# Performance work log

Hardware: AMD Instinct MI355X
Metric: run time of the kernel (lower is better)

## Reference

```python
import jax, jax.numpy as jnp
import numpy as np

INPUT_DIM = 1024
HIDDEN_DIM = 1024
FORGET_BIAS = 0.0


def setup_inputs() -> dict:
    key = jax.random.key(0)
    ks = jax.random.split(key, 8)
    x = jax.random.normal(ks[0], (1024, 32, INPUT_DIM), dtype=jnp.float32)
    state = jnp.zeros((1, 32, HIDDEN_DIM), dtype=jnp.float32)
    std = 0.1
    wm_z = std * jax.random.normal(ks[1], (HIDDEN_DIM, INPUT_DIM), dtype=jnp.float32)
    wm_f = std * jax.random.normal(ks[2], (HIDDEN_DIM, INPUT_DIM), dtype=jnp.float32)
    wv_z = std * jax.random.normal(ks[3], (1, HIDDEN_DIM), dtype=jnp.float32)
    wv_f = std * jax.random.normal(ks[4], (1, HIDDEN_DIM), dtype=jnp.float32)
    bias_z = std * jax.random.normal(ks[5], (1, HIDDEN_DIM), dtype=jnp.float32)
    bias_f = std * jax.random.normal(ks[6], (1, HIDDEN_DIM), dtype=jnp.float32) + FORGET_BIAS
    return {"x": x, "state": state, "wm_z": wm_z, "wm_f": wm_f,
            "wv_z": wv_z, "wv_f": wv_f, "bias_z": bias_z, "bias_f": bias_f}


def reference(x, state, wm_z, wm_f, wv_z, wv_f, bias_z, bias_f):
    # x: [slen, bsz, in_dim]; state: [1, bsz, hidden]
    hidden_prev = state[0]  # [bsz, hidden]
    # Pre-activation input projections (batched GEMM over all timesteps).
    out_z = jnp.einsum('sbi,hi->sbh', x, wm_z)  # [slen, bsz, hidden]
    out_f = jnp.einsum('sbi,hi->sbh', x, wm_f)

    def step(cell, zf):
        z_, f_ = zf
        z_part = jnp.tanh(z_ + wv_z * cell + bias_z)
        f_part = jax.nn.sigmoid(f_ + wv_f * cell + bias_f)
        new_cell = cell * f_part + (1.0 - f_part) * z_part
        return new_cell, new_cell

    _, new_cells = jax.lax.scan(step, hidden_prev, (out_z, out_f))
    return new_cells  # [slen, bsz, hidden]
```

## Files before the change

### kernel.cpp

```cpp
#include <hip/hip_runtime.h>
#include <hip/hip_fp16.h>

#define S_LEN 1024
#define BSZ   32
#define IN_DIM 1024
#define HID   1024
#define MDIM  (S_LEN*BSZ)
#define NDIM  (2*HID)
#define KDIM  IN_DIM

typedef __attribute__((ext_vector_type(8))) _Float16 half8;
typedef __attribute__((ext_vector_type(2))) _Float16 half2v;
typedef __attribute__((ext_vector_type(4))) float    floatx4;

__global__ void cvt_x_kernel(const float* __restrict__ x, _Float16* __restrict__ xh) {
    int idx = blockIdx.x * blockDim.x + threadIdx.x;
    const float4* src = (const float4*)x + (size_t)idx * 2;
    float4 a = src[0], b = src[1];
    half8 h;
    h[0] = (_Float16)a.x; h[1] = (_Float16)a.y; h[2] = (_Float16)a.z; h[3] = (_Float16)a.w;
    h[4] = (_Float16)b.x; h[5] = (_Float16)b.y; h[6] = (_Float16)b.z; h[7] = (_Float16)b.w;
    *((half8*)xh + idx) = h;
}

__global__ void cvt_w_kernel(const float* __restrict__ wz, const float* __restrict__ wf,
                             _Float16* __restrict__ wh) {
    int idx = blockIdx.x * blockDim.x + threadIdx.x;
    int e0 = idx * 8;
    int r   = e0 >> 10;
    int col = e0 & 1023;
    int g = r >> 5, sub = r & 31;
    const float* src = (sub < 16)
        ? wz + ((size_t)(g * 16 + sub)      * KDIM + col)
        : wf + ((size_t)(g * 16 + sub - 16) * KDIM + col);
    const float4* s4 = (const float4*)src;
    float4 a = s4[0], b = s4[1];
    half8 h;
    h[0] = (_Float16)a.x; h[1] = (_Float16)a.y; h[2] = (_Float16)a.z; h[3] = (_Float16)a.w;
    h[4] = (_Float16)b.x; h[5] = (_Float16)b.y; h[6] = (_Float16)b.z; h[7] = (_Float16)b.w;
    *((half8*)wh + idx) = h;
}

#define BM 256
#define BN 256
#define BK 64
#define TPB 4
#define NGT (TPB * 16)
#define NIT (NGT / 2)

__global__ __launch_bounds__(512, 2) void gemm_f16_kernel(
    const _Float16* __restrict__ A, const _Float16* __restrict__ B,
    uint* __restrict__ zf) {
    __shared__ __attribute__((aligned(128))) _Float16 smem[65536];
    char* smb = (char*)smem;

    const int tid  = threadIdx.x;
    const int lane = tid & 63;
    const int wv   = tid >> 6;
    const int wm_off = (wv >> 2) * 128;
    const int wn_off = (wv & 3) * 64;

    const int n0g  = (blockIdx.x & 7) * BN;
    const int m_bs = (blockIdx.x >> 3) * (TPB * BM);

    const int fr  = lane & 15;
    const int fkb = (lane >> 4) * 16;

    const int srow = lane >> 3;
    const int skb  = ((lane & 7) ^ srow) << 4;

    floatx4 acc[8][4] = {};

    auto STAGE_A = [&](int g, int R0) {
        int kt = g & 15, mt = (g >> 4) & 3;
        int r = R0 + wv * 8 + srow;
        const _Float16* gp = A + (size_t)(m_bs + mt * BM + r) * KDIM + kt * BK + (skb >> 1);
        __builtin_amdgcn_global_load_lds(
            (const __attribute__((address_space(1))) void*)gp,
            (__attribute__((address_space(3))) void*)(smb + (g & 1) * 65536 + (R0 + wv * 8) * 128),
            16, 0, 0);
    };
    auto STAGE_B = [&](int g, int R0) {
        int kt = g & 15;
        int r = R0 + wv * 8 + srow;
        const _Float16* gp = B + (size_t)(n0g + r) * KDIM + kt * BK + (skb >> 1);
        __builtin_amdgcn_global_load_lds(
            (const __attribute__((address_space(1))) void*)gp,
            (__attribute__((address_space(3))) void*)(smb + (g & 1) * 65536 + 32768 + (R0 + wv * 8) * 128),
            16, 0, 0);
    };
    auto LD8 = [&](int rb, int r, int kb) -> half8 {
        return *(const half8*)(smb + rb + r * 128 + (kb ^ ((r & 7) << 4)));
    };

    STAGE_B(0, 0);   STAGE_B(0, 64);
    STAGE_A(0, 0);   STAGE_A(0, 128);
    STAGE_B(0, 128); STAGE_B(0, 192);
    STAGE_A(0, 64);  STAGE_A(0, 192);
    STAGE_B(1, 0);   STAGE_B(1, 64);
    STAGE_A(1, 0);   STAGE_A(1, 128);
    STAGE_B(1, 128); STAGE_B(1, 192);
    asm volatile("s_waitcnt vmcnt(6)" ::: "memory");
    __builtin_amdgcn_s_barrier();
    asm volatile("" ::: "memory");

    half8 bfr[4][2];
    for (int it = 0; it < NIT; ++it) {
        const int  t    = 2 * it;
        const bool more = (it < NIT - 1);
        #pragma unroll
        for (int ph = 0; ph < 8; ++ph) {
            const int bb    = ph >> 2;
            const int p     = ph & 3;
            const int bbase = bb * 65536;

            if (p == 0) {
                #pragma unroll
                for (int j = 0; j < 4; ++j)
                    #pragma unroll
                    for (int ks = 0; ks < 2; ++ks) {
                        int r = wn_off + j * 16 + fr;
                        bfr[j][ks] = LD8(bbase + 32768, r, ks * 64 + fkb);
                    }
            }
            half8 afr[2][2];
            #pragma unroll
            for (int ii = 0; ii < 2; ++ii)
                #pragma unroll
                for (int ks = 0; ks < 2; ++ks) {
                    int r = wm_off + (2 * p + ii) * 16 + fr;
                    afr[ii][ks] = LD8(bbase, r, ks * 64 + fkb);
                }

            if (ph == 0) {
                STAGE_A(t + 1, 64);  STAGE_A(t + 1, 192);
            } else if (more) {
                if      (ph == 1) { STAGE_B(t + 2, 0);   STAGE_B(t + 2, 64);  }
                else if (ph == 2) { STAGE_A(t + 2, 0);   STAGE_A(t + 2, 128); }
                else if (ph == 3) { STAGE_B(t + 2, 128); STAGE_B(t + 2, 192); }
                else if (ph == 4) { STAGE_A(t + 2, 64);  STAGE_A(t + 2, 192); }
                else if (ph == 5) { STAGE_B(t + 3, 0);   STAGE_B(t + 3, 64);  }
                else if (ph == 6) { STAGE_A(t + 3, 0);   STAGE_A(t + 3, 128); }
                else              { STAGE_B(t + 3, 128); STAGE_B(t + 3, 192); }
            }

            __builtin_amdgcn_s_barrier();
            asm volatile("s_waitcnt lgkmcnt(0)" ::: "memory");
            __builtin_amdgcn_s_setprio(1);
            #pragma unroll
            for (int ks = 0; ks < 2; ++ks)
                #pragma unroll
                for (int ii = 0; ii < 2; ++ii)
                    #pragma unroll
                    for (int j = 0; j < 4; ++j)
                        acc[2 * p + ii][j] = __builtin_amdgcn_mfma_f32_16x16x32_f16(
                            afr[ii][ks], bfr[j][ks], acc[2 * p + ii][j], 0, 0, 0);
            __builtin_amdgcn_s_setprio(0);
            if (ph == 3) {
                if (more) asm volatile("s_waitcnt vmcnt(6)" ::: "memory");
                else      asm volatile("s_waitcnt vmcnt(0)" ::: "memory");
            } else if (ph == 7) {
                if (more) asm volatile("s_waitcnt vmcnt(6)" ::: "memory");
            }
            __builtin_amdgcn_s_barrier();
            asm volatile("" ::: "memory");
        }

        if ((it & 7) == 7) {
            const int m0   = m_bs + (it >> 3) * BM;
            const int orow = (lane >> 4) * 4;
            const int ocol = lane & 15;
            const int gb   = (n0g + wn_off) >> 5;
            #pragma unroll
            for (int i = 0; i < 8; ++i)
                #pragma unroll
                for (int p2 = 0; p2 < 2; ++p2) {
                    int hh = (gb + p2) * 16 + ocol;
                    #pragma unroll
                    for (int r = 0; r < 4; ++r) {
                        int row = m0 + wm_off + i * 16 + orow + r;
                        half2v v;
                        v[0] = (_Float16)acc[i][2 * p2][r];
                        v[1] = (_Float16)acc[i][2 * p2 + 1][r];
                        *(half2v*)(zf + (size_t)row * HID + hh) = v;
                    }
                }
            #pragma unroll
            for (int i = 0; i < 8; ++i)
                #pragma unroll
                for (int j = 0; j < 4; ++j)
                    acc[i][j] = (floatx4)0.0f;
        }
    }
}

#define UNR 32
__device__ __forceinline__ float fast_exp2(float x) {
    float r;
    asm("v_exp_f32 %0, %1" : "=v"(r) : "v"(x));
    return r;
}
__global__ __launch_bounds__(64) void scan_kernel(
    const uint* __restrict__ zf, float* __restrict__ out,
    const float* __restrict__ state,
    const float* __restrict__ wvz, const float* __restrict__ wvf,
    const float* __restrict__ bz, const float* __restrict__ bfv) {
    const int t = blockIdx.x * 64 + threadIdx.x;
    const int h = t & (HID - 1);
    const int stride = BSZ * HID;

    float cell = state[t];
    const float L2E = 1.44269504088896f;
    const float azt = 2.0f * L2E * wvz[h];
    const float czt = 2.0f * L2E * bz[h];
    const float aft = -L2E * wvf[h];
    const float cft = -L2E * bfv[h];

    const uint* p = zf + t;
    float* po = out + t;

    uint buf[UNR];
    #pragma unroll
    for (int u = 0; u < UNR; ++u) buf[u] = p[(size_t)u * stride];

    for (int s0 = 0; s0 < S_LEN; s0 += UNR) {
        uint nb[UNR];
        if (s0 + UNR < S_LEN) {
            #pragma unroll
            for (int u = 0; u < UNR; ++u)
                nb[u] = p[(size_t)(s0 + UNR + u) * stride];
        }
        #pragma unroll
        for (int u = 0; u < UNR; ++u) {
            half2v h2 = __builtin_bit_cast(half2v, buf[u]);
            float zb = fmaf((float)h2[0], 2.0f * L2E, czt);
            float fb = fmaf((float)h2[1], -L2E, cft);
            float ez = fast_exp2(fmaf(azt, cell, zb));
            float zp = fmaf(-2.0f, __builtin_amdgcn_rcpf(ez + 1.0f), 1.0f);
            float ef = fast_exp2(fmaf(aft, cell, fb));
            float fp = __builtin_amdgcn_rcpf(ef + 1.0f);
            cell = fmaf(cell - zp, fp, zp);
            po[(size_t)(s0 + u) * stride] = cell;
        }
        #pragma unroll
        for (int u = 0; u < UNR; ++u) buf[u] = nb[u];
    }
}

extern "C" void kernel_launch(void* const* d_in, const int* in_sizes, int n_in,
                              void* d_out, int out_size, void* d_ws, size_t ws_size,
                              hipStream_t stream) {
    const float* x      = (const float*)d_in[0];
    const float* state  = (const float*)d_in[1];
    const float* wm_z   = (const float*)d_in[2];
    const float* wm_f   = (const float*)d_in[3];
    const float* wv_z   = (const float*)d_in[4];
    const float* wv_f   = (const float*)d_in[5];
    const float* bias_z = (const float*)d_in[6];
    const float* bias_f = (const float*)d_in[7];
    float* out = (float*)d_out;

    char* ws = (char*)d_ws;
    _Float16* xh = (_Float16*)ws;
    _Float16* wh = (_Float16*)(ws + (size_t)MDIM * KDIM * sizeof(_Float16));
    uint* zf     = (uint*)(ws + (size_t)MDIM * KDIM * sizeof(_Float16)
                              + (size_t)NDIM * KDIM * sizeof(_Float16));

    cvt_x_kernel<<<(MDIM * KDIM) / (256 * 8), 256, 0, stream>>>(x, xh);
    cvt_w_kernel<<<(NDIM * KDIM) / (256 * 8), 256, 0, stream>>>(wm_z, wm_f, wh);

    gemm_f16_kernel<<<256, 512, 0, stream>>>(xh, wh, zf);

    scan_kernel<<<MDIM / 64, 64, 0, stream>>>(zf, out, state, wv_z, wv_f, bias_z, bias_f);
}
```

Measured before the change: 425.1 us.

## Switch GEMM to 32x32x16 MFMA, fuse convert kernels, remap block order

Replaces the 16x16x32 MFMA tiles with 32x32x16 MFMA, which needs fewer LDS fragment reads per flop, and relayouts the interleaved z/f weight rows into 32-row groups to match. The x and weight fp32-to-fp16 conversions are merged into one launch to drop a kernel launch. The block-to-tile mapping now walks the N dimension in the outer index, so concurrently running blocks share the same B tile. Changing the accumulator layout and epilogue indexing risks mismatches with the zf packing the scan kernel expects.

```diff
diff --git a/kernel.cpp b/kernel.cpp
--- a/kernel.cpp
+++ b/kernel.cpp
@@ -9,36 +9,38 @@
 #define NDIM  (2*HID)
 #define KDIM  IN_DIM
 
-typedef __attribute__((ext_vector_type(8))) _Float16 half8;
-typedef __attribute__((ext_vector_type(2))) _Float16 half2v;
-typedef __attribute__((ext_vector_type(4))) float    floatx4;
-
-__global__ void cvt_x_kernel(const float* __restrict__ x, _Float16* __restrict__ xh) {
+typedef __attribute__((ext_vector_type(8)))  _Float16 half8;
+typedef __attribute__((ext_vector_type(2)))  _Float16 half2v;
+typedef __attribute__((ext_vector_type(4)))  float    floatx4;
+typedef __attribute__((ext_vector_type(16))) float    floatx16;
+
+#define NXV ((MDIM*KDIM)/8)
+__global__ void cvt_xw_kernel(const float* __restrict__ x,
+                              const float* __restrict__ wz, const float* __restrict__ wf,
+                              _Float16* __restrict__ xh, _Float16* __restrict__ wh) {
     int idx = blockIdx.x * blockDim.x + threadIdx.x;
-    const float4* src = (const float4*)x + (size_t)idx * 2;
-    float4 a = src[0], b = src[1];
-    half8 h;
-    h[0] = (_Float16)a.x; h[1] = (_Float16)a.y; h[2] = (_Float16)a.z; h[3] = (_Float16)a.w;
-    h[4] = (_Float16)b.x; h[5] = (_Float16)b.y; h[6] = (_Float16)b.z; h[7] = (_Float16)b.w;
-    *((half8*)xh + idx) = h;
-}
-
-__global__ void cvt_w_kernel(const float* __restrict__ wz, const float* __restrict__ wf,
-                             _Float16* __restrict__ wh) {
-    int idx = blockIdx.x * blockDim.x + threadIdx.x;
-    int e0 = idx * 8;
-    int r   = e0 >> 10;
-    int col = e0 & 1023;
-    int g = r >> 5, sub = r & 31;
-    const float* src = (sub < 16)
-        ? wz + ((size_t)(g * 16 + sub)      * KDIM + col)
-        : wf + ((size_t)(g * 16 + sub - 16) * KDIM + col);
-    const float4* s4 = (const float4*)src;
+    const float4* s4;
+    half8* dst;
+    if (idx < NXV) {
+        s4 = (const float4*)x + (size_t)idx * 2;
+        dst = (half8*)xh + idx;
+    } else {
+        int wi = idx - NXV;
+        int e0 = wi * 8;
+        int r   = e0 >> 10;
+        int col = e0 & 1023;
+        int g = r >> 6, sub = r & 63;
+        const float* src = (sub < 32)
+            ? wz + ((size_t)(g * 32 + sub)      * KDIM + col)
+            : wf + ((size_t)(g * 32 + sub - 32) * KDIM + col);
+        s4 = (const float4*)src;
+        dst = (half8*)wh + wi;
+    }
     float4 a = s4[0], b = s4[1];
     half8 h;
     h[0] = (_Float16)a.x; h[1] = (_Float16)a.y; h[2] = (_Float16)a.z; h[3] = (_Float16)a.w;
     h[4] = (_Float16)b.x; h[5] = (_Float16)b.y; h[6] = (_Float16)b.z; h[7] = (_Float16)b.w;
-    *((half8*)wh + idx) = h;
+    *dst = h;
 }
 
 #define BM 256
@@ -60,16 +62,18 @@
     const int wm_off = (wv >> 2) * 128;
     const int wn_off = (wv & 3) * 64;
 
-    const int n0g  = (blockIdx.x & 7) * BN;
-    const int m_bs = (blockIdx.x >> 3) * (TPB * BM);
-
-    const int fr  = lane & 15;
-    const int fkb = (lane >> 4) * 16;
+    const int b      = blockIdx.x;
+    const int mchunk = (b & 7) + 8 * ((b >> 3) & 3);
+    const int m_bs   = mchunk * (TPB * BM);
+    const int n0g    = (b >> 5) * BN;
+
+    const int frow = lane & 31;
+    const int fkb2 = (lane >> 5) * 16;
 
     const int srow = lane >> 3;
     const int skb  = ((lane & 7) ^ srow) << 4;
 
-    floatx4 acc[8][4] = {};
+    floatx16 acc[4][2] = {};
 
     auto STAGE_A = [&](int g, int R0) {
         int kt = g & 15, mt = (g >> 4) & 3;
@@ -104,7 +108,7 @@
     __builtin_amdgcn_s_barrier();
     asm volatile("" ::: "memory");
 
-    half8 bfr[4][2];
+    half8 bfr[2][4];
     for (int it = 0; it < NIT; ++it) {
         const int  t    = 2 * it;
         const bool more = (it < NIT - 1);
@@ -116,21 +120,16 @@
 
             if (p == 0) {
                 #pragma unroll
-                for (int j = 0; j < 4; ++j)
+                for (int nt = 0; nt < 2; ++nt)
                     #pragma unroll
-                    for (int ks = 0; ks < 2; ++ks) {
-                        int r = wn_off + j * 16 + fr;
-                        bfr[j][ks] = LD8(bbase + 32768, r, ks * 64 + fkb);
-                    }
+                    for (int ks = 0; ks < 4; ++ks)
+                        bfr[nt][ks] = LD8(bbase + 32768, wn_off + nt * 32 + frow,
+                                          ks * 32 + fkb2);
             }
-            half8 afr[2][2];
-            #pragma unroll
-            for (int ii = 0; ii < 2; ++ii)
-                #pragma unroll
-                for (int ks = 0; ks < 2; ++ks) {
-                    int r = wm_off + (2 * p + ii) * 16 + fr;
-                    afr[ii][ks] = LD8(bbase, r, ks * 64 + fkb);
-                }
+            half8 afr[4];
+            #pragma unroll
+            for (int ks = 0; ks < 4; ++ks)
+                afr[ks] = LD8(bbase, wm_off + p * 32 + frow, ks * 32 + fkb2);
 
             if (ph == 0) {
                 STAGE_A(t + 1, 64);  STAGE_A(t + 1, 192);
@@ -148,13 +147,11 @@
             asm volatile("s_waitcnt lgkmcnt(0)" ::: "memory");
             __builtin_amdgcn_s_setprio(1);
             #pragma unroll
-            for (int ks = 0; ks < 2; ++ks)
-                #pragma unroll
-                for (int ii = 0; ii < 2; ++ii)
-                    #pragma unroll
-                    for (int j = 0; j < 4; ++j)
-                        acc[2 * p + ii][j] = __builtin_amdgcn_mfma_f32_16x16x32_f16(
-                            afr[ii][ks], bfr[j][ks], acc[2 * p + ii][j], 0, 0, 0);
+            for (int ks = 0; ks < 4; ++ks)
+                #pragma unroll
+                for (int nt = 0; nt < 2; ++nt)
+                    acc[p][nt] = __builtin_amdgcn_mfma_f32_32x32x16_f16(
+                        afr[ks], bfr[nt][ks], acc[p][nt], 0, 0, 0);
             __builtin_amdgcn_s_setprio(0);
             if (ph == 3) {
                 if (more) asm volatile("s_waitcnt vmcnt(6)" ::: "memory");
@@ -167,29 +164,25 @@
         }
 
         if ((it & 7) == 7) {
-            const int m0   = m_bs + (it >> 3) * BM;
-            const int orow = (lane >> 4) * 4;
-            const int ocol = lane & 15;
-            const int gb   = (n0g + wn_off) >> 5;
-            #pragma unroll
-            for (int i = 0; i < 8; ++i)
-                #pragma unroll
-                for (int p2 = 0; p2 < 2; ++p2) {
-                    int hh = (gb + p2) * 16 + ocol;
-                    #pragma unroll
-                    for (int r = 0; r < 4; ++r) {
-                        int row = m0 + wm_off + i * 16 + orow + r;
-                        half2v v;
-                        v[0] = (_Float16)acc[i][2 * p2][r];
-                        v[1] = (_Float16)acc[i][2 * p2 + 1][r];
-                        *(half2v*)(zf + (size_t)row * HID + hh) = v;
-                    }
+            const int m0    = m_bs + (it >> 3) * BM;
+            const int rbase = (lane >> 5) * 4;
+            const int hcol  = lane & 31;
+            const int hb    = (n0g + wn_off) >> 1;
+            #pragma unroll
+            for (int mt = 0; mt < 4; ++mt)
+                #pragma unroll
+                for (int q = 0; q < 16; ++q) {
+                    int row = m0 + wm_off + mt * 32 + (q & 3) + 8 * (q >> 2) + rbase;
+                    half2v v;
+                    v[0] = (_Float16)acc[mt][0][q];
+                    v[1] = (_Float16)acc[mt][1][q];
+                    *(half2v*)(zf + (size_t)row * HID + hb + hcol) = v;
                 }
             #pragma unroll
-            for (int i = 0; i < 8; ++i)
-                #pragma unroll
-                for (int j = 0; j < 4; ++j)
-                    acc[i][j] = (floatx4)0.0f;
+            for (int i = 0; i < 4; ++i)
+                #pragma unroll
+                for (int j = 0; j < 2; ++j)
+                    acc[i][j] = (floatx16)0.0f;
         }
     }
 }
@@ -266,8 +259,8 @@
     uint* zf     = (uint*)(ws + (size_t)MDIM * KDIM * sizeof(_Float16)
                               + (size_t)NDIM * KDIM * sizeof(_Float16));
 
-    cvt_x_kernel<<<(MDIM * KDIM) / (256 * 8), 256, 0, stream>>>(x, xh);
-    cvt_w_kernel<<<(NDIM * KDIM) / (256 * 8), 256, 0, stream>>>(wm_z, wm_f, wh);
+    cvt_xw_kernel<<<((MDIM + NDIM) * KDIM) / (256 * 8), 256, 0, stream>>>(
+        x, wm_z, wm_f, xh, wh);
 
     gemm_f16_kernel<<<256, 512, 0, stream>>>(xh, wh, zf);
 
```

Result: slower. 445.6 us (+4.8%).
